# Performance work log

Hardware: AMD Instinct MI355X
Metric: run time of the kernel (lower is better)

The kernel has to match this reference:

```python
import jax, jax.numpy as jnp
import numpy as np
from jax import lax

B, L, C = 8, 1024, 256
H = 8  # num_heads
EPS = 1e-5


def _conv_bn(img, w, gamma, beta):
    # img: [B, C_in, h, w]; w: [C_out, C_in, 3, 3]; 3x3 conv, stride 1, pad 1, no bias
    out = lax.conv_general_dilated(img, w, window_strides=(1, 1),
                                   padding=[(1, 1), (1, 1)],
                                   dimension_numbers=('NCHW', 'OIHW', 'NCHW'))
    # BatchNorm2d in train mode: per-channel batch stats over (B, h, w), biased var
    mu = out.mean(axis=(0, 2, 3), keepdims=True)
    var = out.var(axis=(0, 2, 3), keepdims=True)
    out = (out - mu) * lax.rsqrt(var + EPS)
    out = out * gamma[None, :, None, None] + beta[None, :, None, None]
    b, c, hh, ww = out.shape
    return out.reshape(b, c, hh * ww).transpose(0, 2, 1)  # b (h w) c


def setup_inputs() -> dict:
    key = jax.random.key(0)
    ks = jax.random.split(key, 10)
    s = 0.02
    inp = {
        'x': jax.random.normal(ks[0], (B, L, C), jnp.float32),
        'y': jax.random.normal(ks[1], (B, L, C), jnp.float32),
        'h': 32,
        'w': 32,
        'conv_q_w': jax.random.normal(ks[2], (C, C, 3, 3), jnp.float32) * s,
        'bn_q_g': jnp.ones((C,), jnp.float32),
        'bn_q_b': jnp.zeros((C,), jnp.float32),
        'conv_k_w': jax.random.normal(ks[3], (C, C, 3, 3), jnp.float32) * s,
        'bn_k_g': jnp.ones((C,), jnp.float32),
        'bn_k_b': jnp.zeros((C,), jnp.float32),
        'conv_v_w': jax.random.normal(ks[4], (C, C, 3, 3), jnp.float32) * s,
        'bn_v_g': jnp.ones((C,), jnp.float32),
        'bn_v_b': jnp.zeros((C,), jnp.float32),
        'Wq': jax.random.normal(ks[5], (C, C), jnp.float32) * s,
        'Wk': jax.random.normal(ks[6], (C, C), jnp.float32) * s,
        'Wv': jax.random.normal(ks[7], (C, C), jnp.float32) * s,
        'Wo': jax.random.normal(ks[8], (C, C), jnp.float32) * s,
        'bo': jnp.zeros((C,), jnp.float32),
    }
    return inp


def reference(x, y, h, w,
              conv_q_w, bn_q_g, bn_q_b,
              conv_k_w, bn_k_g, bn_k_b,
              conv_v_w, bn_v_g, bn_v_b,
              Wq, Wk, Wv, Wo, bo):
    b, t, c = x.shape
    x_img = x.transpose(0, 2, 1).reshape(b, c, h, w)
    y_img = y.transpose(0, 2, 1).reshape(b, c, h, w)

    q = _conv_bn(x_img, conv_q_w, bn_q_g, bn_q_b)  # [B, L, C]
    k = _conv_bn(y_img, conv_k_w, bn_k_g, bn_k_b)
    v = _conv_bn(y_img, conv_v_w, bn_v_g, bn_v_b)

    d = c // H
    # Linear (no bias) then split heads: b t (h d) -> b h t d
    q = (q @ Wq.T).reshape(b, -1, H, d).transpose(0, 2, 1, 3)
    k = (k @ Wk.T).reshape(b, -1, H, d).transpose(0, 2, 1, 3)
    v = (v @ Wv.T).reshape(b, -1, H, d).transpose(0, 2, 1, 3)

    scale = c ** (-0.5)  # NOTE: original scales by dim_q**-0.5, not head_dim
    attn = jax.nn.softmax(jnp.einsum('bhlk,bhtk->bhlt', q, k) * scale, axis=-1)
    out = jnp.einsum('bhlt,bhtv->bhlv', attn, v)
    out = out.transpose(0, 2, 1, 3).reshape(b, -1, c)  # b h t d -> b t (h d)
    return out @ Wo.T + bo
```

## Files before the change

### kernel.cpp

```cpp
#include <hip/hip_runtime.h>
#include <cmath>

#define BB 8
#define LLEN 1024
#define CC 256
#define NH 8
#define HD 32
#define IMG 32
#define EPSBN 1e-5f
#define QSCALE 0.0625f
#define SCLOG2E 0.09016844005556f

typedef short bf16x8 __attribute__((ext_vector_type(8)));
typedef short bf16x4 __attribute__((ext_vector_type(4)));
typedef float f32x4 __attribute__((ext_vector_type(4)));

static __device__ __forceinline__ unsigned short f2bf(float v) {
  union { float f; unsigned u; } a; a.f = v;
  unsigned r = a.u + 0x7fff + ((a.u >> 16) & 1);
  return (unsigned short)(r >> 16);
}
static __device__ __forceinline__ float bf2f(unsigned short s) {
  union { unsigned u; float f; } a; a.u = ((unsigned)s) << 16; return a.f;
}

__global__ __launch_bounds__(256) void k_prep_xy(const float* __restrict__ x,
                                                 const float* __restrict__ y,
                                                 short* __restrict__ xh,
                                                 short* __restrict__ yh) {
  const float* s = blockIdx.y ? y : x;
  short* d = blockIdx.y ? yh : xh;
  size_t i = (size_t)(blockIdx.x << 8) + threadIdx.x;
  float4 v = ((const float4*)s)[i];
  bf16x4 o;
  o[0] = (short)f2bf(v.x); o[1] = (short)f2bf(v.y);
  o[2] = (short)f2bf(v.z); o[3] = (short)f2bf(v.w);
  *(bf16x4*)(d + i * 4) = o;
}

__global__ __launch_bounds__(256) void k_prep_w(const float* __restrict__ w0,
                                                const float* __restrict__ w1,
                                                const float* __restrict__ w2,
                                                short* __restrict__ Wrh) {
  const float* w = blockIdx.y == 0 ? w0 : (blockIdx.y == 1 ? w1 : w2);
  int co = blockIdx.x, ci = threadIdx.x;
  const float* src = w + ((size_t)co * CC + ci) * 9;
  size_t ob = (size_t)blockIdx.y * 9 * 65536;
#pragma unroll
  for (int tap = 0; tap < 9; ++tap)
    Wrh[ob + (size_t)(tap * CC + co) * CC + ci] = (short)f2bf(src[tap]);
}

__global__ __launch_bounds__(256) void k_prep_wo(const float* __restrict__ Wo,
                                                 short* __restrict__ Woh,
                                                 short* __restrict__ Wol) {
  int i = (blockIdx.x << 8) + threadIdx.x;
  float v = Wo[i];
  unsigned short h = f2bf(v);
  Woh[i] = (short)h;
  Wol[i] = (short)f2bf(v - bf2f(h));
}

__global__ __launch_bounds__(256, 2) void k_conv(const short* __restrict__ xh,
                                                 const short* __restrict__ yh,
                                                 const short* __restrict__ Wrh,
                                                 short* __restrict__ ch,
                                                 float* __restrict__ st) {
  __shared__ __align__(16) short sW[9 * 64 * 32];
  __shared__ __align__(16) short sI[340 * 32];
  __shared__ float sws[4][64];
  __shared__ float swq[4][64];

  int tid = threadIdx.x;
  int co0 = blockIdx.x << 6;
  int r0 = blockIdx.y << 3;
  int z = blockIdx.z;
  int t = z >> 3, b = z & 7;
  const short* inb = (t == 0 ? xh : yh) + (size_t)b * LLEN * CC;
  const short* wb = Wrh + (size_t)t * 9 * 65536;

  int lane = tid & 63, w = tid >> 6;
  int quad = lane >> 4, mm = lane & 15;

  int pbA[4];
#pragma unroll
  for (int mt = 0; mt < 4; ++mt) {
    int sp = w * 64 + mt * 16 + mm;
    pbA[mt] = (sp >> 5) * 34 + (sp & 31);
  }
  const int dtap[9] = {0, 1, 2, 34, 35, 36, 68, 69, 70};

  f32x4 acc[4][4];
#pragma unroll
  for (int mt = 0; mt < 4; ++mt)
#pragma unroll
    for (int nt = 0; nt < 4; ++nt) acc[mt][nt] = (f32x4){0.f, 0.f, 0.f, 0.f};

  for (int kc = 0; kc < 8; ++kc) {
    int ci0 = kc << 5;
    __syncthreads();
#pragma unroll
    for (int j = 0; j < 9; ++j) {
      int idx = tid + (j << 8);
      int tap = idx >> 8;
      int rem = idx & 255;
      int col = rem >> 2, cg = rem & 3;
      bf16x8 v = *(const bf16x8*)(wb + (size_t)tap * 65536 +
                                  (size_t)(co0 + col) * CC + ci0 + cg * 8);
      *(bf16x8*)(sW + tap * 2048 + col * 32 + cg * 8) = v;
    }
#pragma unroll
    for (int j = 0; j < 6; ++j) {
      int idx = tid + (j << 8);
      if (idx < 1360) {
        int sp_p = idx >> 2, cg = idx & 3;
        int pr = sp_p / 34;
        int px = sp_p - pr * 34;
        int ir = r0 - 1 + pr;
        int xx = px - 1;
        bf16x8 v = {0, 0, 0, 0, 0, 0, 0, 0};
        if (ir >= 0 && ir < IMG && xx >= 0 && xx < IMG)
          v = *(const bf16x8*)(inb + (size_t)(ir * 32 + xx) * CC + ci0 + cg * 8);
        *(bf16x8*)(sI + sp_p * 32 + ((cg ^ (sp_p & 3)) << 3)) = v;
      }
    }
    __syncthreads();

#pragma unroll
    for (int tap = 0; tap < 9; ++tap) {
      bf16x8 Af[4], Bw[4];
#pragma unroll
      for (int mt = 0; mt < 4; ++mt) {
        int sp_p = pbA[mt] + dtap[tap];
        Af[mt] = *(const bf16x8*)(sI + sp_p * 32 + ((quad ^ (sp_p & 3)) << 3));
      }
#pragma unroll
      for (int nt = 0; nt < 4; ++nt)
        Bw[nt] = *(const bf16x8*)(sW + tap * 2048 + (nt * 16 + mm) * 32 + quad * 8);
#pragma unroll
      for (int mt = 0; mt < 4; ++mt)
#pragma unroll
        for (int nt = 0; nt < 4; ++nt)
          acc[mt][nt] = __builtin_amdgcn_mfma_f32_16x16x32_bf16(Af[mt], Bw[nt],
                                                                acc[mt][nt], 0, 0, 0);
    }
  }

  size_t tb = (size_t)t * 8192 + b * 1024 + r0 * 32;
#pragma unroll
  for (int mt = 0; mt < 4; ++mt)
#pragma unroll
    for (int nt = 0; nt < 4; ++nt)
#pragma unroll
      for (int r = 0; r < 4; ++r) {
        int sp = w * 64 + mt * 16 + quad * 4 + r;
        ch[(tb + sp) * CC + co0 + nt * 16 + mm] = (short)f2bf(acc[mt][nt][r]);
      }

  float s[4], q[4];
#pragma unroll
  for (int nt = 0; nt < 4; ++nt) {
    float ss = 0.f, qq = 0.f;
#pragma unroll
    for (int mt = 0; mt < 4; ++mt)
#pragma unroll
      for (int r = 0; r < 4; ++r) {
        float v = acc[mt][nt][r];
        ss += v;
        qq += v * v;
      }
    ss += __shfl_xor(ss, 16); ss += __shfl_xor(ss, 32);
    qq += __shfl_xor(qq, 16); qq += __shfl_xor(qq, 32);
    s[nt] = ss; q[nt] = qq;
  }
  if (quad == 0) {
#pragma unroll
    for (int nt = 0; nt < 4; ++nt) {
      sws[w][nt * 16 + mm] = s[nt];
      swq[w][nt * 16 + mm] = q[nt];
    }
  }
  __syncthreads();
  if (tid < 64) {
    float S = sws[0][tid] + sws[1][tid] + sws[2][tid] + sws[3][tid];
    float Q = swq[0][tid] + swq[1][tid] + swq[2][tid] + swq[3][tid];
    atomicAdd(&st[t * 512 + co0 + tid], S);
    atomicAdd(&st[t * 512 + 256 + co0 + tid], Q);
  }
}

__global__ __launch_bounds__(256) void k_fuse(const float* __restrict__ Wq,
                                              const float* __restrict__ Wk,
                                              const float* __restrict__ Wv,
                                              const float* __restrict__ gq,
                                              const float* __restrict__ gk,
                                              const float* __restrict__ gv,
                                              const float* __restrict__ bq,
                                              const float* __restrict__ bk,
                                              const float* __restrict__ bv,
                                              const float* __restrict__ st,
                                              short* __restrict__ Wfh,
                                              short* __restrict__ Wfl,
                                              float* __restrict__ bfv) {
  int t = blockIdx.y;
  const float* W = t == 0 ? Wq : (t == 1 ? Wk : Wv);
  const float* gamma = t == 0 ? gq : (t == 1 ? gk : gv);
  const float* beta = t == 0 ? bq : (t == 1 ? bk : bv);
  int co = blockIdx.x, ci = threadIdx.x;
  float mu = st[t * 512 + ci] * (1.f / 8192.f);
  float var = st[t * 512 + 256 + ci] * (1.f / 8192.f) - mu * mu;
  float a = gamma[ci] * rsqrtf(var + EPSBN);
  float dt = beta[ci] - mu * a;
  float wv = W[co * CC + ci];
  float v = wv * a;
  unsigned short hh = f2bf(v);
  Wfh[(size_t)t * 65536 + co * CC + ci] = (short)hh;
  Wfl[(size_t)t * 65536 + co * CC + ci] = (short)f2bf(v - bf2f(hh));
  __shared__ float red[256];
  red[ci] = dt * wv;
  __syncthreads();
  for (int s2 = 128; s2 > 0; s2 >>= 1) {
    if (ci < s2) red[ci] += red[ci + s2];
    __syncthreads();
  }
  if (ci == 0) bfv[t * 256 + co] = red[0];
}

__global__ __launch_bounds__(256, 2) void k_proj(const short* __restrict__ ch,
                                                 const short* __restrict__ Wfh,
                                                 const short* __restrict__ Wfl,
                                                 const float* __restrict__ bfv,
                                                 short* __restrict__ Qh,
                                                 short* __restrict__ Kh,
                                                 short* __restrict__ Vh) {
  __shared__ __align__(16) short sT[64 * 264];
  int tid = threadIdx.x;
  int t = blockIdx.z;
  int t0 = blockIdx.x << 8;
  int co0 = blockIdx.y << 6;
  int lane = tid & 63, w = tid >> 6;
  int quad = lane >> 4, mm = lane & 15;
  int colw = co0 + w * 16;
  const short* cht = ch + (size_t)t * 8192 * CC;

  bf16x8 Bh[8], Bl[8];
  {
    const short* bh = Wfh + (size_t)t * 65536 + (size_t)(colw + mm) * CC + quad * 8;
    const short* bl = Wfl + (size_t)t * 65536 + (size_t)(colw + mm) * CC + quad * 8;
#pragma unroll
    for (int kc = 0; kc < 8; ++kc) {
      Bh[kc] = *(const bf16x8*)(bh + kc * 32);
      Bl[kc] = *(const bf16x8*)(bl + kc * 32);
    }
  }
  float bv = bfv[t * 256 + colw + mm];

  bf16x8 A0[8], A1[8];
  auto loadA = [&](bf16x8* dst, int g) {
    const short* a = cht + (size_t)(t0 + g * 16 + mm) * CC + quad * 8;
#pragma unroll
    for (int kc = 0; kc < 8; ++kc) dst[kc] = *(const bf16x8*)(a + kc * 32);
  };
  auto compute = [&](const bf16x8* A, int g) {
    f32x4 aH = {0.f, 0.f, 0.f, 0.f}, aL = {0.f, 0.f, 0.f, 0.f};
#pragma unroll
    for (int kc = 0; kc < 8; ++kc) {
      aH = __builtin_amdgcn_mfma_f32_16x16x32_bf16(A[kc], Bh[kc], aH, 0, 0, 0);
      aL = __builtin_amdgcn_mfma_f32_16x16x32_bf16(A[kc], Bl[kc], aL, 0, 0, 0);
    }
    if (t == 0) {
#pragma unroll
      for (int r = 0; r < 4; ++r) {
        int token = t0 + g * 16 + quad * 4 + r;
        Qh[(size_t)token * CC + colw + mm] =
            (short)f2bf((aH[r] + aL[r] + bv) * SCLOG2E);
      }
    } else if (t == 1) {
#pragma unroll
      for (int r = 0; r < 4; ++r) {
        int token = t0 + g * 16 + quad * 4 + r;
        Kh[(size_t)token * CC + colw + mm] = (short)f2bf(aH[r] + aL[r] + bv);
      }
    } else {
#pragma unroll
      for (int r = 0; r < 4; ++r)
        sT[(w * 16 + mm) * 264 + (g >> 2) * 64 + 16 * quad + 4 * r + (g & 3)] =
            (short)f2bf(aH[r] + aL[r] + bv);
    }
  };

  loadA(A0, 0);
#pragma unroll
  for (int g = 0; g < 16; g += 2) {
    loadA(A1, g + 1);
    compute(A0, g);
    if (g + 2 < 16) loadA(A0, g + 2);
    compute(A1, g + 1);
  }

  if (t == 2) {
    __syncthreads();
    int b = t0 >> 10, l0 = t0 & 1023;
#pragma unroll
    for (int j = 0; j < 8; ++j) {
      int idx = tid + (j << 8);
      int co = idx >> 5, tg = idx & 31;
      bf16x8 v = *(const bf16x8*)(sT + co * 264 + tg * 8);
      *(bf16x8*)(Vh + ((size_t)(b * CC) + co0 + co) * LLEN + l0 + tg * 8) = v;
    }
  }
}

__global__ __launch_bounds__(256, 2) void k_attn(const short* __restrict__ Qh,
                                                 const short* __restrict__ Kh,
                                                 const short* __restrict__ Vh,
                                                 short* __restrict__ AOh) {
  __shared__ __align__(16) short sK[64 * 32];
  __shared__ __align__(16) short sV[32 * 72];
  __shared__ __align__(16) short sP[4 * 32 * 72];

  int tid = threadIdx.x;
  int lane = tid & 63, w = tid >> 6;
  int quad = lane >> 4, mm = lane & 15;
  int bh = blockIdx.x;
  int b = bh >> 3, h = bh & 7;
  int l0 = blockIdx.y << 7;

  bf16x8 qf[2];
#pragma unroll
  for (int mf = 0; mf < 2; ++mf)
    qf[mf] = *(const bf16x8*)(Qh + ((size_t)(b * LLEN) + l0 + w * 32 + mf * 16 + mm) * CC +
                              h * HD + quad * 8);

  f32x4 accO[2][2], accL[2];
#pragma unroll
  for (int mf = 0; mf < 2; ++mf) {
    accO[mf][0] = (f32x4){0.f, 0.f, 0.f, 0.f};
    accO[mf][1] = (f32x4){0.f, 0.f, 0.f, 0.f};
    accL[mf] = (f32x4){0.f, 0.f, 0.f, 0.f};
  }
  bf16x8 ones;
#pragma unroll
  for (int j = 0; j < 8; ++j) ones[j] = (short)0x3F80;

  int kt = tid >> 2, kc4 = tid & 3;
  const short* kgp = Kh + ((size_t)(b * LLEN) + kt) * CC + h * HD + kc4 * 8;
  short* kst = sK + kt * 32 + kc4 * 8;
  int vd = tid >> 3, vt8 = tid & 7;
  const short* vgp = Vh + ((size_t)(b * CC) + h * HD + vd) * LLEN + vt8 * 8;
  short* vst = sV + vd * 72 + vt8 * 8;
  short* pw = sP + w * (32 * 72);

  for (int t0 = 0; t0 < LLEN; t0 += 64) {
    __syncthreads();
    *(bf16x8*)kst = *(const bf16x8*)(kgp + (size_t)t0 * CC);
    *(bf16x8*)vst = *(const bf16x8*)(vgp + t0);
    __syncthreads();

#pragma unroll
    for (int mf = 0; mf < 2; ++mf) {
      f32x4 accS[4];
#pragma unroll
      for (int nt = 0; nt < 4; ++nt) {
        bf16x8 kf = *(const bf16x8*)(sK + (nt * 16 + mm) * 32 + quad * 8);
        f32x4 z = {0.f, 0.f, 0.f, 0.f};
        accS[nt] = __builtin_amdgcn_mfma_f32_16x16x32_bf16(qf[mf], kf, z, 0, 0, 0);
      }
#pragma unroll
      for (int r = 0; r < 4; ++r) {
        int q = mf * 16 + quad * 4 + r;
        bf16x4 pk;
#pragma unroll
        for (int nt = 0; nt < 4; ++nt) {
          union { float f; unsigned u; } cv;
          cv.f = __builtin_exp2f(accS[nt][r]);
          pk[nt] = (short)((cv.u + 0x8000u) >> 16);
        }
        *(bf16x4*)(pw + q * 72 + mm * 4) = pk;
      }
    }

#pragma unroll
    for (int kc = 0; kc < 2; ++kc) {
      bf16x8 vf0 = *(const bf16x8*)(sV + mm * 72 + kc * 32 + quad * 8);
      bf16x8 vf1 = *(const bf16x8*)(sV + (16 + mm) * 72 + kc * 32 + quad * 8);
#pragma unroll
      for (int mf = 0; mf < 2; ++mf) {
        bf16x8 pf = *(const bf16x8*)(pw + (mf * 16 + mm) * 72 + kc * 32 + quad * 8);
        accL[mf] = __builtin_amdgcn_mfma_f32_16x16x32_bf16(pf, ones, accL[mf], 0, 0, 0);
        accO[mf][0] = __builtin_amdgcn_mfma_f32_16x16x32_bf16(pf, vf0, accO[mf][0], 0, 0, 0);
        accO[mf][1] = __builtin_amdgcn_mfma_f32_16x16x32_bf16(pf, vf1, accO[mf][1], 0, 0, 0);
      }
    }
  }

#pragma unroll
  for (int mf = 0; mf < 2; ++mf)
#pragma unroll
    for (int r = 0; r < 4; ++r) {
      float inv = __builtin_amdgcn_rcpf(accL[mf][r]);
      size_t token = (size_t)(b * LLEN) + l0 + w * 32 + mf * 16 + quad * 4 + r;
      AOh[token * CC + h * HD + mm] = (short)f2bf(accO[mf][0][r] * inv);
      AOh[token * CC + h * HD + 16 + mm] = (short)f2bf(accO[mf][1][r] * inv);
    }
}

__global__ __launch_bounds__(256, 2) void k_out(const short* __restrict__ AOh,
                                                const short* __restrict__ Woh,
                                                const short* __restrict__ Wol,
                                                const float* __restrict__ bo,
                                                float* __restrict__ out) {
  int tid = threadIdx.x;
  int t0 = blockIdx.x << 7;
  int co0 = blockIdx.y << 6;
  int lane = tid & 63, w = tid >> 6;
  int quad = lane >> 4, mm = lane & 15;
  int colw = co0 + w * 16;

  bf16x8 Bh[8], Bl[8];
  {
    const short* bh = Woh + (size_t)(colw + mm) * CC + quad * 8;
    const short* bl = Wol + (size_t)(colw + mm) * CC + quad * 8;
#pragma unroll
    for (int kc = 0; kc < 8; ++kc) {
      Bh[kc] = *(const bf16x8*)(bh + kc * 32);
      Bl[kc] = *(const bf16x8*)(bl + kc * 32);
    }
  }
  float bv = bo[colw + mm];

  bf16x8 A0[8], A1[8];
  auto loadA = [&](bf16x8* dst, int g) {
    const short* a = AOh + (size_t)(t0 + g * 16 + mm) * CC + quad * 8;
#pragma unroll
    for (int kc = 0; kc < 8; ++kc) dst[kc] = *(const bf16x8*)(a + kc * 32);
  };
  auto compute = [&](const bf16x8* A, int g) {
    f32x4 aH = {0.f, 0.f, 0.f, 0.f}, aL = {0.f, 0.f, 0.f, 0.f};
#pragma unroll
    for (int kc = 0; kc < 8; ++kc) {
      aH = __builtin_amdgcn_mfma_f32_16x16x32_bf16(A[kc], Bh[kc], aH, 0, 0, 0);
      aL = __builtin_amdgcn_mfma_f32_16x16x32_bf16(A[kc], Bl[kc], aL, 0, 0, 0);
    }
#pragma unroll
    for (int r = 0; r < 4; ++r) {
      int token = t0 + g * 16 + quad * 4 + r;
      out[(size_t)token * CC + colw + mm] = aH[r] + aL[r] + bv;
    }
  };

  loadA(A0, 0);
#pragma unroll
  for (int g = 0; g < 8; g += 2) {
    loadA(A1, g + 1);
    compute(A0, g);
    if (g + 2 < 8) loadA(A0, g + 2);
    compute(A1, g + 1);
  }
}

extern "C" void kernel_launch(void* const* d_in, const int* in_sizes, int n_in,
                              void* d_out, int out_size, void* d_ws, size_t ws_size,
                              hipStream_t stream) {
  (void)in_sizes; (void)n_in; (void)out_size; (void)ws_size;
  const float* x  = (const float*)d_in[0];
  const float* y  = (const float*)d_in[1];
  const float* wq = (const float*)d_in[4];
  const float* gq = (const float*)d_in[5];
  const float* bq = (const float*)d_in[6];
  const float* wk = (const float*)d_in[7];
  const float* gk = (const float*)d_in[8];
  const float* bk = (const float*)d_in[9];
  const float* wv = (const float*)d_in[10];
  const float* gv = (const float*)d_in[11];
  const float* bv = (const float*)d_in[12];
  const float* Wq = (const float*)d_in[13];
  const float* Wk = (const float*)d_in[14];
  const float* Wv = (const float*)d_in[15];
  const float* Wo = (const float*)d_in[16];
  const float* bo = (const float*)d_in[17];
  float* out = (float*)d_out;

  const size_t NP = (size_t)8192 * 256;
  short* xh  = (short*)d_ws;
  short* yh  = xh + NP;
  short* ch  = yh + NP;
  short* Qh  = ch + 3 * NP;
  short* Kh  = Qh + NP;
  short* Vh  = Kh + NP;
  short* AOh = Vh + NP;
  short* Wrh = AOh + NP;
  short* Wfh = Wrh + (size_t)3 * 9 * 65536;
  short* Wfl = Wfh + 3 * 65536;
  short* Woh = Wfl + 3 * 65536;
  short* Wol = Woh + 65536;
  float* st  = (float*)(Wol + 65536);
  float* bfv = st + 1536;

  hipMemsetAsync(st, 0, 1536 * sizeof(float), stream);

  k_prep_xy<<<dim3(2048, 2), 256, 0, stream>>>(x, y, xh, yh);
  k_prep_w<<<dim3(256, 3), 256, 0, stream>>>(wq, wk, wv, Wrh);
  k_prep_wo<<<256, 256, 0, stream>>>(Wo, Woh, Wol);

  k_conv<<<dim3(4, 4, 24), 256, 0, stream>>>(xh, yh, Wrh, ch, st);

  k_fuse<<<dim3(256, 3), 256, 0, stream>>>(Wq, Wk, Wv, gq, gk, gv, bq, bk, bv,
                                           st, Wfh, Wfl, bfv);

  k_proj<<<dim3(32, 4, 3), 256, 0, stream>>>(ch, Wfh, Wfl, bfv, Qh, Kh, Vh);

  k_attn<<<dim3(64, 8), 256, 0, stream>>>(Qh, Kh, Vh, AOh);

  k_out<<<dim3(64, 4), 256, 0, stream>>>(AOh, Woh, Wol, bo, out);
}
```

Baseline: 219.4 us.

## Merge prep kernels, load conv weights from global, double-buffer attention K/V

Three separate weight/input conversion kernels become one launch, which removes two kernel launches. The conv kernel stops staging weights in shared memory and reads B fragments straight from global/L2, freeing LDS so occupancy can rise to 3 blocks. The attention kernel double-buffers its K/V tiles, prefetching the next tile into registers during compute. Direct global weight loads may raise memory latency in the conv inner loop, and the attention loop still keeps two barriers per iteration.

```diff
diff --git a/kernel.cpp b/kernel.cpp
--- a/kernel.cpp
+++ b/kernel.cpp
@@ -24,49 +24,50 @@
   union { unsigned u; float f; } a; a.u = ((unsigned)s) << 16; return a.f;
 }
 
-__global__ __launch_bounds__(256) void k_prep_xy(const float* __restrict__ x,
-                                                 const float* __restrict__ y,
-                                                 short* __restrict__ xh,
-                                                 short* __restrict__ yh) {
-  const float* s = blockIdx.y ? y : x;
-  short* d = blockIdx.y ? yh : xh;
-  size_t i = (size_t)(blockIdx.x << 8) + threadIdx.x;
-  float4 v = ((const float4*)s)[i];
-  bf16x4 o;
-  o[0] = (short)f2bf(v.x); o[1] = (short)f2bf(v.y);
-  o[2] = (short)f2bf(v.z); o[3] = (short)f2bf(v.w);
-  *(bf16x4*)(d + i * 4) = o;
-}
-
-__global__ __launch_bounds__(256) void k_prep_w(const float* __restrict__ w0,
-                                                const float* __restrict__ w1,
-                                                const float* __restrict__ w2,
-                                                short* __restrict__ Wrh) {
-  const float* w = blockIdx.y == 0 ? w0 : (blockIdx.y == 1 ? w1 : w2);
-  int co = blockIdx.x, ci = threadIdx.x;
-  const float* src = w + ((size_t)co * CC + ci) * 9;
-  size_t ob = (size_t)blockIdx.y * 9 * 65536;
-#pragma unroll
-  for (int tap = 0; tap < 9; ++tap)
-    Wrh[ob + (size_t)(tap * CC + co) * CC + ci] = (short)f2bf(src[tap]);
-}
-
-__global__ __launch_bounds__(256) void k_prep_wo(const float* __restrict__ Wo,
-                                                 short* __restrict__ Woh,
-                                                 short* __restrict__ Wol) {
-  int i = (blockIdx.x << 8) + threadIdx.x;
-  float v = Wo[i];
-  unsigned short h = f2bf(v);
-  Woh[i] = (short)h;
-  Wol[i] = (short)f2bf(v - bf2f(h));
-}
-
-__global__ __launch_bounds__(256, 2) void k_conv(const short* __restrict__ xh,
+__global__ __launch_bounds__(256) void k_prep(const float* __restrict__ x,
+                                              const float* __restrict__ y,
+                                              const float* __restrict__ w0,
+                                              const float* __restrict__ w1,
+                                              const float* __restrict__ w2,
+                                              const float* __restrict__ Wo,
+                                              short* __restrict__ xh,
+                                              short* __restrict__ yh,
+                                              short* __restrict__ Wrh,
+                                              short* __restrict__ Woh,
+                                              short* __restrict__ Wol) {
+  int bid = blockIdx.x;
+  if (bid < 4096) {
+    const float* s = bid >= 2048 ? y : x;
+    short* d = bid >= 2048 ? yh : xh;
+    size_t i = (size_t)((bid & 2047) << 8) + threadIdx.x;
+    float4 v = ((const float4*)s)[i];
+    bf16x4 o;
+    o[0] = (short)f2bf(v.x); o[1] = (short)f2bf(v.y);
+    o[2] = (short)f2bf(v.z); o[3] = (short)f2bf(v.w);
+    *(bf16x4*)(d + i * 4) = o;
+  } else if (bid < 4864) {
+    int k = bid - 4096;
+    int t = k >> 8, co = k & 255, ci = threadIdx.x;
+    const float* w = t == 0 ? w0 : (t == 1 ? w1 : w2);
+    const float* src = w + ((size_t)co * CC + ci) * 9;
+    size_t ob = (size_t)t * 9 * 65536;
+#pragma unroll
+    for (int tap = 0; tap < 9; ++tap)
+      Wrh[ob + (size_t)(tap * CC + co) * CC + ci] = (short)f2bf(src[tap]);
+  } else {
+    int i = ((bid - 4864) << 8) + threadIdx.x;
+    float v = Wo[i];
+    unsigned short h = f2bf(v);
+    Woh[i] = (short)h;
+    Wol[i] = (short)f2bf(v - bf2f(h));
+  }
+}
+
+__global__ __launch_bounds__(256, 3) void k_conv(const short* __restrict__ xh,
                                                  const short* __restrict__ yh,
                                                  const short* __restrict__ Wrh,
                                                  short* __restrict__ ch,
                                                  float* __restrict__ st) {
-  __shared__ __align__(16) short sW[9 * 64 * 32];
   __shared__ __align__(16) short sI[340 * 32];
   __shared__ float sws[4][64];
   __shared__ float swq[4][64];
@@ -90,6 +91,8 @@
   }
   const int dtap[9] = {0, 1, 2, 34, 35, 36, 68, 69, 70};
 
+  const short* wbase = wb + (size_t)(co0 + mm) * CC + quad * 8;
+
   f32x4 acc[4][4];
 #pragma unroll
   for (int mt = 0; mt < 4; ++mt)
@@ -99,16 +102,6 @@
   for (int kc = 0; kc < 8; ++kc) {
     int ci0 = kc << 5;
     __syncthreads();
-#pragma unroll
-    for (int j = 0; j < 9; ++j) {
-      int idx = tid + (j << 8);
-      int tap = idx >> 8;
-      int rem = idx & 255;
-      int col = rem >> 2, cg = rem & 3;
-      bf16x8 v = *(const bf16x8*)(wb + (size_t)tap * 65536 +
-                                  (size_t)(co0 + col) * CC + ci0 + cg * 8);
-      *(bf16x8*)(sW + tap * 2048 + col * 32 + cg * 8) = v;
-    }
 #pragma unroll
     for (int j = 0; j < 6; ++j) {
       int idx = tid + (j << 8);
@@ -126,17 +119,19 @@
     }
     __syncthreads();
 
+    const short* wk0 = wbase + ci0;
 #pragma unroll
     for (int tap = 0; tap < 9; ++tap) {
-      bf16x8 Af[4], Bw[4];
+      bf16x8 Bw[4];
+#pragma unroll
+      for (int nt = 0; nt < 4; ++nt)
+        Bw[nt] = *(const bf16x8*)(wk0 + (size_t)tap * 65536 + nt * 4096);
+      bf16x8 Af[4];
 #pragma unroll
       for (int mt = 0; mt < 4; ++mt) {
         int sp_p = pbA[mt] + dtap[tap];
         Af[mt] = *(const bf16x8*)(sI + sp_p * 32 + ((quad ^ (sp_p & 3)) << 3));
       }
-#pragma unroll
-      for (int nt = 0; nt < 4; ++nt)
-        Bw[nt] = *(const bf16x8*)(sW + tap * 2048 + (nt * 16 + mm) * 32 + quad * 8);
 #pragma unroll
       for (int mt = 0; mt < 4; ++mt)
 #pragma unroll
@@ -315,8 +310,8 @@
                                                  const short* __restrict__ Kh,
                                                  const short* __restrict__ Vh,
                                                  short* __restrict__ AOh) {
-  __shared__ __align__(16) short sK[64 * 32];
-  __shared__ __align__(16) short sV[32 * 72];
+  __shared__ __align__(16) short sK[2][64 * 32];
+  __shared__ __align__(16) short sV[2][32 * 72];
   __shared__ __align__(16) short sP[4 * 32 * 72];
 
   int tid = threadIdx.x;
@@ -345,24 +340,32 @@
 
   int kt = tid >> 2, kc4 = tid & 3;
   const short* kgp = Kh + ((size_t)(b * LLEN) + kt) * CC + h * HD + kc4 * 8;
-  short* kst = sK + kt * 32 + kc4 * 8;
+  int kofs = kt * 32 + kc4 * 8;
   int vd = tid >> 3, vt8 = tid & 7;
   const short* vgp = Vh + ((size_t)(b * CC) + h * HD + vd) * LLEN + vt8 * 8;
-  short* vst = sV + vd * 72 + vt8 * 8;
+  int vofs = vd * 72 + vt8 * 8;
   short* pw = sP + w * (32 * 72);
 
-  for (int t0 = 0; t0 < LLEN; t0 += 64) {
-    __syncthreads();
-    *(bf16x8*)kst = *(const bf16x8*)(kgp + (size_t)t0 * CC);
-    *(bf16x8*)vst = *(const bf16x8*)(vgp + t0);
-    __syncthreads();
+  bf16x8 kr = *(const bf16x8*)kgp;
+  bf16x8 vr = *(const bf16x8*)vgp;
+  *(bf16x8*)(sK[0] + kofs) = kr;
+  *(bf16x8*)(sV[0] + vofs) = vr;
+  __syncthreads();
+
+  for (int tt = 0; tt < 16; ++tt) {
+    if (tt < 15) {
+      kr = *(const bf16x8*)(kgp + (size_t)(tt + 1) * 64 * CC);
+      vr = *(const bf16x8*)(vgp + (tt + 1) * 64);
+    }
+    const short* sKc = sK[tt & 1];
+    const short* sVc = sV[tt & 1];
 
 #pragma unroll
     for (int mf = 0; mf < 2; ++mf) {
       f32x4 accS[4];
 #pragma unroll
       for (int nt = 0; nt < 4; ++nt) {
-        bf16x8 kf = *(const bf16x8*)(sK + (nt * 16 + mm) * 32 + quad * 8);
+        bf16x8 kf = *(const bf16x8*)(sKc + (nt * 16 + mm) * 32 + quad * 8);
         f32x4 z = {0.f, 0.f, 0.f, 0.f};
         accS[nt] = __builtin_amdgcn_mfma_f32_16x16x32_bf16(qf[mf], kf, z, 0, 0, 0);
       }
@@ -382,8 +385,8 @@
 
 #pragma unroll
     for (int kc = 0; kc < 2; ++kc) {
-      bf16x8 vf0 = *(const bf16x8*)(sV + mm * 72 + kc * 32 + quad * 8);
-      bf16x8 vf1 = *(const bf16x8*)(sV + (16 + mm) * 72 + kc * 32 + quad * 8);
+      bf16x8 vf0 = *(const bf16x8*)(sVc + mm * 72 + kc * 32 + quad * 8);
+      bf16x8 vf1 = *(const bf16x8*)(sVc + (16 + mm) * 72 + kc * 32 + quad * 8);
 #pragma unroll
       for (int mf = 0; mf < 2; ++mf) {
         bf16x8 pf = *(const bf16x8*)(pw + (mf * 16 + mm) * 72 + kc * 32 + quad * 8);
@@ -391,6 +394,13 @@
         accO[mf][0] = __builtin_amdgcn_mfma_f32_16x16x32_bf16(pf, vf0, accO[mf][0], 0, 0, 0);
         accO[mf][1] = __builtin_amdgcn_mfma_f32_16x16x32_bf16(pf, vf1, accO[mf][1], 0, 0, 0);
       }
+    }
+
+    if (tt < 15) {
+      __syncthreads();
+      *(bf16x8*)(sK[(tt + 1) & 1] + kofs) = kr;
+      *(bf16x8*)(sV[(tt + 1) & 1] + vofs) = vr;
+      __syncthreads();
     }
   }
 
@@ -499,9 +509,7 @@
 
   hipMemsetAsync(st, 0, 1536 * sizeof(float), stream);
 
-  k_prep_xy<<<dim3(2048, 2), 256, 0, stream>>>(x, y, xh, yh);
-  k_prep_w<<<dim3(256, 3), 256, 0, stream>>>(wq, wk, wv, Wrh);
-  k_prep_wo<<<256, 256, 0, stream>>>(Wo, Woh, Wol);
+  k_prep<<<5120, 256, 0, stream>>>(x, y, wq, wk, wv, Wo, xh, yh, Wrh, Woh, Wol);
 
   k_conv<<<dim3(4, 4, 24), 256, 0, stream>>>(xh, yh, Wrh, ch, st);
 
```

Result: slower. 255.9 us (+16.7%).
